# Kernel tuning notes

Measured on AMD Instinct MI355X. Metric: run time of the kernel, lower is better.

## Reference

```python
import jax, jax.numpy as jnp
import numpy as np


def setup_inputs() -> dict:
    key = jax.random.key(0)
    ks = jax.random.split(key, 8)
    B, C, T = 8, 512, 2048
    Cq = C // 8
    s = 0.02
    return {
        "x": jax.random.normal(ks[0], (B, C, T), dtype=jnp.float32),
        "wq": jax.random.normal(ks[1], (Cq, C), dtype=jnp.float32) * s,
        "bq": jax.random.normal(ks[2], (Cq,), dtype=jnp.float32) * s,
        "wk": jax.random.normal(ks[3], (Cq, C), dtype=jnp.float32) * s,
        "bk": jax.random.normal(ks[4], (Cq,), dtype=jnp.float32) * s,
        "wv": jax.random.normal(ks[5], (C, C), dtype=jnp.float32) * s,
        "bv": jax.random.normal(ks[6], (C,), dtype=jnp.float32) * s,
        "gamma": jax.random.normal(ks[7], (1,), dtype=jnp.float32) * s,
    }


def reference(x, wq, bq, wk, bk, wv, bv, gamma):
    # x: [B, C, T]; conv1d with kernel_size=1 == per-timestep linear over channels
    q = jnp.einsum('oc,bct->bto', wq, x) + bq          # [B, T, Cq]
    k = jnp.einsum('oc,bct->bot', wk, x) + bk[None, :, None]  # [B, Cq, T]
    v = jnp.einsum('oc,bct->bto', wv, x) + bv          # [B, T, C]
    attn = jnp.einsum('bto,bos->bts', q, k)            # [B, T, T] (unscaled)
    attn = jax.nn.softmax(attn, axis=-1)
    out = jnp.einsum('bts,bsc->bct', attn, v)          # [B, C, T]
    return gamma[0] * out + x
```

## Files before the change

kernel.cpp:

```cpp
#include <hip/hip_runtime.h>


#define B_ 8
#define C_ 512
#define T_ 2048

typedef __attribute__((ext_vector_type(4))) float f32x4;
typedef __attribute__((ext_vector_type(8))) short bf16x8;
typedef unsigned short u16;
typedef unsigned int u32;

__device__ __forceinline__ u16 f2bf(float f) {
  u32 u = __float_as_uint(f);
  u += 0x7fffu + ((u >> 16) & 1);
  return (u16)(u >> 16);
}
__device__ __forceinline__ float bf2f(u16 h) {
  return __uint_as_float(((u32)h) << 16);
}

extern "C" __global__ __launch_bounds__(256)
void k_wcvt(const float* __restrict__ wq, const float* __restrict__ wk,
            const float* __restrict__ wv, u16* __restrict__ W) {
  int i = blockIdx.x * 256 + threadIdx.x;
  const float* src; u16* dst;
  if (i < 8192)       { src = wq + (size_t)i * 4;            dst = W + (size_t)i * 4; }
  else if (i < 16384) { int j = i - 8192;  src = wk + (size_t)j * 4; dst = W + 32768 + (size_t)j * 4; }
  else                { int j = i - 16384; src = wv + (size_t)j * 4; dst = W + 65536 + (size_t)j * 4; }
  float4 f = *(const float4*)src;
  ushort4 o;
  o.x = f2bf(f.x); o.y = f2bf(f.y); o.z = f2bf(f.z); o.w = f2bf(f.w);
  *(ushort4*)dst = o;
}

extern "C" __global__ __launch_bounds__(256)
void k_xpose(const float* __restrict__ x, u16* __restrict__ xT) {
  __shared__ alignas(16) u16 lds[64 * 72];
  const int tid = threadIdx.x;
  const int t0 = blockIdx.x * 64;
  const int c0 = blockIdx.y * 64;
  const int b  = blockIdx.z;
  const int cr = tid >> 2, tq = tid & 3;
  const float* xp = x + ((size_t)(b * C_ + c0 + cr)) * T_ + t0 + tq * 16;
  u16 vals[16];
#pragma unroll
  for (int q = 0; q < 4; q++) {
    float4 f = *(const float4*)(xp + q * 4);
    vals[q * 4 + 0] = f2bf(f.x);
    vals[q * 4 + 1] = f2bf(f.y);
    vals[q * 4 + 2] = f2bf(f.z);
    vals[q * 4 + 3] = f2bf(f.w);
  }
#pragma unroll
  for (int j = 0; j < 16; j++) lds[(tq * 16 + j) * 72 + cr] = vals[j];
  __syncthreads();
  const int tr = tid >> 2, cq = tid & 3;
  uint4 oa = *(const uint4*)&lds[tr * 72 + cq * 16];
  uint4 ob = *(const uint4*)&lds[tr * 72 + cq * 16 + 8];
  u16* op = xT + ((size_t)(b * T_ + t0 + tr)) * C_ + c0 + cq * 16;
  *(uint4*)op = oa;
  *(uint4*)(op + 8) = ob;
}

extern "C" __global__ __launch_bounds__(256)
void k_qk(const u16* __restrict__ xT, const u16* __restrict__ W,
          const float* __restrict__ bq, const float* __restrict__ bk,
          u16* __restrict__ QK) {
  const int tid = threadIdx.x;
  const int wave = tid >> 6, lane = tid & 63;
  const int quad = lane >> 4, l15 = lane & 15;
  const int id = blockIdx.x;
  const int b  = id & 7;
  const int t0 = (id >> 3) * 32;
  const int n0 = wave * 32;
  f32x4 acc[2][2];
#pragma unroll
  for (int i = 0; i < 2; i++)
#pragma unroll
    for (int j = 0; j < 2; j++) acc[i][j] = (f32x4){0.f, 0.f, 0.f, 0.f};
#pragma unroll
  for (int ks = 0; ks < 16; ks++) {
    bf16x8 af[2], bf[2];
#pragma unroll
    for (int mt = 0; mt < 2; mt++)
      af[mt] = *(const bf16x8*)(xT + ((size_t)(b * T_ + t0 + mt * 16 + l15)) * C_ +
                                ks * 32 + quad * 8);
#pragma unroll
    for (int ntl = 0; ntl < 2; ntl++) {
      const int n = n0 + ntl * 16 + l15;
      const u16* wrow = (n < 64) ? (W + (size_t)n * C_)
                                 : (W + 32768 + (size_t)(n - 64) * C_);
      bf[ntl] = *(const bf16x8*)(wrow + ks * 32 + quad * 8);
    }
#pragma unroll
    for (int mt = 0; mt < 2; mt++)
#pragma unroll
      for (int ntl = 0; ntl < 2; ntl++)
        acc[mt][ntl] = __builtin_amdgcn_mfma_f32_16x16x32_bf16(af[mt], bf[ntl],
                                                               acc[mt][ntl], 0, 0, 0);
  }
#pragma unroll
  for (int ntl = 0; ntl < 2; ntl++) {
    const int n = n0 + ntl * 16 + l15;
    const float bias = (n < 64) ? bq[n] : bk[n - 64];
#pragma unroll
    for (int mt = 0; mt < 2; mt++)
#pragma unroll
      for (int r = 0; r < 4; r++) {
        const int t = t0 + mt * 16 + quad * 4 + r;
        QK[((size_t)(b * T_ + t)) * 128 + n] = f2bf(acc[mt][ntl][r] + bias);
      }
  }
}

extern "C" __global__ __launch_bounds__(256)
void k_vt(const u16* __restrict__ xT, const u16* __restrict__ Wv,
          const float* __restrict__ bv, u16* __restrict__ VT) {
  const int tid = threadIdx.x;
  const int wave = tid >> 6, lane = tid & 63;
  const int quad = lane >> 4, l15 = lane & 15;
  const int id = blockIdx.x;
  const int b   = id & 7;
  const int slot = id >> 3;
  const int tt0 = (slot & 15) * 128;
  const int c00 = (slot >> 4) * 128;
  const int wm = (wave >> 1) * 64, wn = (wave & 1) * 64;
  f32x4 acc[4][4];
#pragma unroll
  for (int i = 0; i < 4; i++)
#pragma unroll
    for (int j = 0; j < 4; j++) acc[i][j] = (f32x4){0.f, 0.f, 0.f, 0.f};

  bf16x8 af[2][4], bfr[2][4];
  auto ldst = [&](int ks, int s) {
#pragma unroll
    for (int mt = 0; mt < 4; mt++)
      af[s][mt] = *(const bf16x8*)(Wv + ((size_t)(c00 + wm + mt * 16 + l15)) * C_ +
                                   ks * 32 + quad * 8);
#pragma unroll
    for (int nt = 0; nt < 4; nt++)
      bfr[s][nt] = *(const bf16x8*)(xT + ((size_t)(b * T_ + tt0 + wn + nt * 16 + l15)) * C_ +
                                    ks * 32 + quad * 8);
  };
  ldst(0, 0);
#pragma unroll
  for (int ks = 0; ks < 16; ks++) {
    const int cur = ks & 1;
    if (ks < 15) ldst(ks + 1, cur ^ 1);
#pragma unroll
    for (int mt = 0; mt < 4; mt++)
#pragma unroll
      for (int nt = 0; nt < 4; nt++)
        acc[mt][nt] = __builtin_amdgcn_mfma_f32_16x16x32_bf16(af[cur][mt], bfr[cur][nt],
                                                              acc[mt][nt], 0, 0, 0);
  }
#pragma unroll
  for (int mt = 0; mt < 4; mt++) {
#pragma unroll
    for (int r = 0; r < 4; r++) {
      const int c = c00 + wm + mt * 16 + quad * 4 + r;
      const float bias = bv[c];
#pragma unroll
      for (int nt = 0; nt < 4; nt++) {
        const int t = tt0 + wn + nt * 16 + l15;
        VT[((size_t)(b * C_ + c)) * T_ + t] = f2bf(acc[mt][nt][r] + bias);
      }
    }
  }
}

extern "C" __global__ __launch_bounds__(256)
void k_attn(const u16* __restrict__ QK, const u16* __restrict__ VT,
            const float* __restrict__ x, const float* __restrict__ gamma,
            float* __restrict__ out) {
  __shared__ alignas(16) u16 Vt[2][128 * 88];
  __shared__ alignas(16) u16 Pscr[4][32 * 64];

  const int tid = threadIdx.x;
  const int wave = tid >> 6, lane = tid & 63;
  const int quad = lane >> 4, l15 = lane & 15;
  const int id = blockIdx.x;
  const int b  = id & 7;
  const int slot = id >> 3;
  const int c0 = (slot >> 4) * 128;
  const int t0 = (slot & 15) * 128;
  const int t0w = t0 + wave * 32;

  bf16x8 qa[2][2];
#pragma unroll
  for (int mt = 0; mt < 2; mt++) {
    const u16* qp = QK + ((size_t)(b * T_ + t0w + mt * 16 + l15)) * 128 + quad * 8;
    qa[mt][0] = *(const bf16x8*)qp;
    qa[mt][1] = *(const bf16x8*)(qp + 32);
  }
  f32x4 acc[2][8];
#pragma unroll
  for (int i = 0; i < 2; i++)
#pragma unroll
    for (int j = 0; j < 8; j++) acc[i][j] = (f32x4){0.f, 0.f, 0.f, 0.f};
  f32x4 acc1[2];
  acc1[0] = (f32x4){0.f, 0.f, 0.f, 0.f};
  acc1[1] = (f32x4){0.f, 0.f, 0.f, 0.f};
  bf16x8 ones;
#pragma unroll
  for (int j = 0; j < 8; j++) ones[j] = (short)0x3F80;

  const u16* vbase = VT + ((size_t)(b * C_ + c0)) * T_;
  const u16* kp = QK + ((size_t)(b * T_ + l15)) * 128 + 64 + quad * 8;

  const int vrow = tid >> 1, vh = tid & 1;
  uint4 vreg[4];
  auto gl_v = [&](int s0) {
    const u16* p = vbase + (size_t)vrow * T_ + s0 + vh * 32;
    vreg[0] = *(const uint4*)p;
    vreg[1] = *(const uint4*)(p + 8);
    vreg[2] = *(const uint4*)(p + 16);
    vreg[3] = *(const uint4*)(p + 24);
  };
  auto st_v = [&](int par) {
    u16* d = &Vt[par][vrow * 88 + vh * 32];
    *(uint4*)(d)      = vreg[0];
    *(uint4*)(d + 8)  = vreg[1];
    *(uint4*)(d + 16) = vreg[2];
    *(uint4*)(d + 24) = vreg[3];
  };

  bf16x8 kbf[4][2];
  auto ld_k = [&](int s0) {
#pragma unroll
    for (int nt = 0; nt < 4; nt++)
#pragma unroll
      for (int ks = 0; ks < 2; ks++)
        kbf[nt][ks] = *(const bf16x8*)(kp + (size_t)((s0 + nt * 16) << 7) + ks * 32);
  };

  ld_k(0);
  gl_v(0);
  st_v(0);
  __syncthreads();

  for (int i = 0; i < 32; i++) {
    const int par = i & 1;
    if (i < 31) gl_v((i + 1) * 64);

    f32x4 sacc[2][4];
#pragma unroll
    for (int mt = 0; mt < 2; mt++)
#pragma unroll
      for (int nt = 0; nt < 4; nt++) sacc[mt][nt] = (f32x4){0.f, 0.f, 0.f, 0.f};
#pragma unroll
    for (int nt = 0; nt < 4; nt++)
#pragma unroll
      for (int ks = 0; ks < 2; ks++)
#pragma unroll
        for (int mt = 0; mt < 2; mt++)
          sacc[mt][nt] = __builtin_amdgcn_mfma_f32_16x16x32_bf16(qa[mt][ks], kbf[nt][ks],
                                                                 sacc[mt][nt], 0, 0, 0);

    if (i < 31) ld_k((i + 1) * 64);

#pragma unroll
    for (int mt = 0; mt < 2; mt++)
#pragma unroll
      for (int nt = 0; nt < 4; nt++) {
        float p0 = __expf(sacc[mt][nt][0]);
        float p1 = __expf(sacc[mt][nt][1]);
        float p2 = __expf(sacc[mt][nt][2]);
        float p3 = __expf(sacc[mt][nt][3]);
        u32 w01, w23;
        asm("v_cvt_pk_bf16_f32 %0, %1, %2" : "=v"(w01) : "v"(p0), "v"(p1));
        asm("v_cvt_pk_bf16_f32 %0, %1, %2" : "=v"(w23) : "v"(p2), "v"(p3));
        const u16 h[4] = {(u16)w01, (u16)(w01 >> 16), (u16)w23, (u16)(w23 >> 16)};
        const int sH = (nt << 1) | (l15 >> 3);
        const int sL = l15 & 7;
#pragma unroll
        for (int r = 0; r < 4; r++) {
          const int tl = mt * 16 + quad * 4 + r;
          Pscr[wave][tl * 64 + ((sH ^ (tl & 7)) << 3) + sL] = h[r];
        }
      }
    bf16x8 pa[2][2];
#pragma unroll
    for (int mt = 0; mt < 2; mt++)
#pragma unroll
      for (int sb = 0; sb < 2; sb++) {
        const int tl = mt * 16 + l15;
        const int sl = ((sb * 4 + quad) ^ (tl & 7)) << 3;
        pa[mt][sb] = *(const bf16x8*)&Pscr[wave][tl * 64 + sl];
      }

#pragma unroll
    for (int mt = 0; mt < 2; mt++)
#pragma unroll
      for (int sb = 0; sb < 2; sb++)
        acc1[mt] = __builtin_amdgcn_mfma_f32_16x16x32_bf16(pa[mt][sb], ones,
                                                           acc1[mt], 0, 0, 0);

#pragma unroll
    for (int nt = 0; nt < 8; nt++)
#pragma unroll
      for (int sb = 0; sb < 2; sb++) {
        bf16x8 vb = *(const bf16x8*)&Vt[par][(nt * 16 + l15) * 88 + sb * 32 + quad * 8];
#pragma unroll
        for (int mt = 0; mt < 2; mt++)
          acc[mt][nt] = __builtin_amdgcn_mfma_f32_16x16x32_bf16(pa[mt][sb], vb,
                                                                acc[mt][nt], 0, 0, 0);
      }

    if (i < 31) st_v(par ^ 1);
    __syncthreads();
  }

  const float g = gamma[0];
#pragma unroll
  for (int mt = 0; mt < 2; mt++) {
#pragma unroll
    for (int r = 0; r < 4; r++) {
      const int t = t0w + mt * 16 + quad * 4 + r;
      const float sc = g / acc1[mt][r];
#pragma unroll
      for (int nt = 0; nt < 8; nt++) {
        const int c = c0 + nt * 16 + l15;
        const size_t idx = ((size_t)(b * C_ + c)) * T_ + t;
        out[idx] = acc[mt][nt][r] * sc + x[idx];
      }
    }
  }
}

extern "C" void kernel_launch(void* const* d_in, const int* in_sizes, int n_in,
                              void* d_out, int out_size, void* d_ws, size_t ws_size,
                              hipStream_t stream) {
  (void)in_sizes; (void)n_in; (void)out_size; (void)ws_size;
  const float* x  = (const float*)d_in[0];
  const float* wq = (const float*)d_in[1];
  const float* bq = (const float*)d_in[2];
  const float* wk = (const float*)d_in[3];
  const float* bk = (const float*)d_in[4];
  const float* wv = (const float*)d_in[5];
  const float* bv = (const float*)d_in[6];
  const float* gm = (const float*)d_in[7];
  float* out = (float*)d_out;

  u16* xT = (u16*)d_out;
  u16* Wb = (u16*)((char*)d_out + (size_t)17 * 1024 * 1024);
  char* ws = (char*)d_ws;
  u16* QK = (u16*)ws;
  u16* VT = (u16*)(ws + (size_t)4 * 1024 * 1024);

  k_wcvt<<<320, 256, 0, stream>>>(wq, wk, wv, Wb);
  k_xpose<<<dim3(32, 8, 8), 256, 0, stream>>>(x, xT);
  k_qk  <<<512, 256, 0, stream>>>(xT, Wb, bq, bk, QK);
  k_vt  <<<512, 256, 0, stream>>>(xT, Wb + 65536, bv, VT);
  k_attn<<<512, 256, 0, stream>>>(QK, VT, x, gm, out);
}
```

Measured before the change: 257.0 us.

## Switch attention to 32x32x16 MFMA with transposed S and register-resident P

Rewrites the attention kernel around 32x32x16 bf16 MFMAs. S is computed transposed (K as the A operand) so that the exp'd probabilities can be repacked into B-operand fragments in registers with v_permlane32_swap, which removes the per-wave LDS scratch round trip for P. The row-sum now accumulates in a scalar plus one cross-half shuffle instead of extra MFMAs against a ones vector. The V tile in LDS drops its padding in favour of an XOR swizzle. Together these cut LDS traffic and instruction count, but the larger accumulators raise register pressure and the output stores change their access pattern.

```diff
diff --git a/kernel.cpp b/kernel.cpp
--- a/kernel.cpp
+++ b/kernel.cpp
@@ -6,6 +6,7 @@
 #define T_ 2048
 
 typedef __attribute__((ext_vector_type(4))) float f32x4;
+typedef __attribute__((ext_vector_type(16))) float f32x16;
 typedef __attribute__((ext_vector_type(8))) short bf16x8;
 typedef unsigned short u16;
 typedef unsigned int u32;
@@ -173,12 +174,11 @@
 void k_attn(const u16* __restrict__ QK, const u16* __restrict__ VT,
             const float* __restrict__ x, const float* __restrict__ gamma,
             float* __restrict__ out) {
-  __shared__ alignas(16) u16 Vt[2][128 * 88];
-  __shared__ alignas(16) u16 Pscr[4][32 * 64];
+  __shared__ alignas(16) u16 Vt[2][128 * 64];
 
   const int tid = threadIdx.x;
   const int wave = tid >> 6, lane = tid & 63;
-  const int quad = lane >> 4, l15 = lane & 15;
+  const int l31 = lane & 31, lh = lane >> 5;
   const int id = blockIdx.x;
   const int b  = id & 7;
   const int slot = id >> 3;
@@ -186,27 +186,21 @@
   const int t0 = (slot & 15) * 128;
   const int t0w = t0 + wave * 32;
 
-  bf16x8 qa[2][2];
-#pragma unroll
-  for (int mt = 0; mt < 2; mt++) {
-    const u16* qp = QK + ((size_t)(b * T_ + t0w + mt * 16 + l15)) * 128 + quad * 8;
-    qa[mt][0] = *(const bf16x8*)qp;
-    qa[mt][1] = *(const bf16x8*)(qp + 32);
-  }
-  f32x4 acc[2][8];
-#pragma unroll
-  for (int i = 0; i < 2; i++)
-#pragma unroll
-    for (int j = 0; j < 8; j++) acc[i][j] = (f32x4){0.f, 0.f, 0.f, 0.f};
-  f32x4 acc1[2];
-  acc1[0] = (f32x4){0.f, 0.f, 0.f, 0.f};
-  acc1[1] = (f32x4){0.f, 0.f, 0.f, 0.f};
-  bf16x8 ones;
-#pragma unroll
-  for (int j = 0; j < 8; j++) ones[j] = (short)0x3F80;
+  bf16x8 qf[4];
+  {
+    const u16* qq = QK + ((size_t)(b * T_ + t0w + l31)) * 128 + lh * 8;
+#pragma unroll
+    for (int kc = 0; kc < 4; kc++)
+      qf[kc] = *(const bf16x8*)(qq + kc * 16);
+  }
+
+  f32x16 acc[4];
+#pragma unroll
+  for (int ct = 0; ct < 4; ct++) acc[ct] = {};
+  float lacc = 0.f;
 
   const u16* vbase = VT + ((size_t)(b * C_ + c0)) * T_;
-  const u16* kp = QK + ((size_t)(b * T_ + l15)) * 128 + 64 + quad * 8;
+  const u16* kq = QK + ((size_t)(b * T_ + l31)) * 128 + 64 + lh * 8;
 
   const int vrow = tid >> 1, vh = tid & 1;
   uint4 vreg[4];
@@ -218,20 +212,19 @@
     vreg[3] = *(const uint4*)(p + 24);
   };
   auto st_v = [&](int par) {
-    u16* d = &Vt[par][vrow * 88 + vh * 32];
-    *(uint4*)(d)      = vreg[0];
-    *(uint4*)(d + 8)  = vreg[1];
-    *(uint4*)(d + 16) = vreg[2];
-    *(uint4*)(d + 24) = vreg[3];
+    u16* row = &Vt[par][vrow * 64];
+#pragma unroll
+    for (int k = 0; k < 4; k++)
+      *(uint4*)(row + (((vh * 4 + k) ^ (vrow & 7)) << 3)) = vreg[k];
   };
 
-  bf16x8 kbf[4][2];
+  bf16x8 kbf[2][4];
   auto ld_k = [&](int s0) {
 #pragma unroll
-    for (int nt = 0; nt < 4; nt++)
-#pragma unroll
-      for (int ks = 0; ks < 2; ks++)
-        kbf[nt][ks] = *(const bf16x8*)(kp + (size_t)((s0 + nt * 16) << 7) + ks * 32);
+    for (int nt = 0; nt < 2; nt++)
+#pragma unroll
+      for (int kc = 0; kc < 4; kc++)
+        kbf[nt][kc] = *(const bf16x8*)(kq + (size_t)((s0 + nt * 32) << 7) + kc * 16);
   };
 
   ld_k(0);
@@ -243,87 +236,65 @@
     const int par = i & 1;
     if (i < 31) gl_v((i + 1) * 64);
 
-    f32x4 sacc[2][4];
-#pragma unroll
-    for (int mt = 0; mt < 2; mt++)
-#pragma unroll
-      for (int nt = 0; nt < 4; nt++) sacc[mt][nt] = (f32x4){0.f, 0.f, 0.f, 0.f};
-#pragma unroll
-    for (int nt = 0; nt < 4; nt++)
-#pragma unroll
-      for (int ks = 0; ks < 2; ks++)
-#pragma unroll
-        for (int mt = 0; mt < 2; mt++)
-          sacc[mt][nt] = __builtin_amdgcn_mfma_f32_16x16x32_bf16(qa[mt][ks], kbf[nt][ks],
-                                                                 sacc[mt][nt], 0, 0, 0);
+    bf16x8 pf[4];
+#pragma unroll
+    for (int nt = 0; nt < 2; nt++) {
+      f32x16 s = {};
+#pragma unroll
+      for (int kc = 0; kc < 4; kc++)
+        s = __builtin_amdgcn_mfma_f32_32x32x16_bf16(kbf[nt][kc], qf[kc], s, 0, 0, 0);
+      float p[16];
+#pragma unroll
+      for (int r = 0; r < 16; r++) {
+        p[r] = __expf(s[r]);
+        lacc += p[r];
+      }
+#pragma unroll
+      for (int g = 0; g < 2; g++) {
+        const float* pp = p + g * 8;
+        u32 A, Bv, Cv, Dv;
+        asm("v_cvt_pk_bf16_f32 %0, %1, %2" : "=v"(A)  : "v"(pp[0]), "v"(pp[1]));
+        asm("v_cvt_pk_bf16_f32 %0, %1, %2" : "=v"(Bv) : "v"(pp[2]), "v"(pp[3]));
+        asm("v_cvt_pk_bf16_f32 %0, %1, %2" : "=v"(Cv) : "v"(pp[4]), "v"(pp[5]));
+        asm("v_cvt_pk_bf16_f32 %0, %1, %2" : "=v"(Dv) : "v"(pp[6]), "v"(pp[7]));
+        asm("v_permlane32_swap_b32 %0, %1" : "+v"(A), "+v"(Cv));
+        asm("v_permlane32_swap_b32 %0, %1" : "+v"(Bv), "+v"(Dv));
+        union { bf16x8 v; u32 w[4]; } u;
+        u.w[0] = A; u.w[1] = Bv; u.w[2] = Cv; u.w[3] = Dv;
+        pf[nt * 2 + g] = u.v;
+      }
+    }
 
     if (i < 31) ld_k((i + 1) * 64);
 
 #pragma unroll
-    for (int mt = 0; mt < 2; mt++)
-#pragma unroll
-      for (int nt = 0; nt < 4; nt++) {
-        float p0 = __expf(sacc[mt][nt][0]);
-        float p1 = __expf(sacc[mt][nt][1]);
-        float p2 = __expf(sacc[mt][nt][2]);
-        float p3 = __expf(sacc[mt][nt][3]);
-        u32 w01, w23;
-        asm("v_cvt_pk_bf16_f32 %0, %1, %2" : "=v"(w01) : "v"(p0), "v"(p1));
-        asm("v_cvt_pk_bf16_f32 %0, %1, %2" : "=v"(w23) : "v"(p2), "v"(p3));
-        const u16 h[4] = {(u16)w01, (u16)(w01 >> 16), (u16)w23, (u16)(w23 >> 16)};
-        const int sH = (nt << 1) | (l15 >> 3);
-        const int sL = l15 & 7;
-#pragma unroll
-        for (int r = 0; r < 4; r++) {
-          const int tl = mt * 16 + quad * 4 + r;
-          Pscr[wave][tl * 64 + ((sH ^ (tl & 7)) << 3) + sL] = h[r];
-        }
-      }
-    bf16x8 pa[2][2];
-#pragma unroll
-    for (int mt = 0; mt < 2; mt++)
-#pragma unroll
-      for (int sb = 0; sb < 2; sb++) {
-        const int tl = mt * 16 + l15;
-        const int sl = ((sb * 4 + quad) ^ (tl & 7)) << 3;
-        pa[mt][sb] = *(const bf16x8*)&Pscr[wave][tl * 64 + sl];
-      }
-
-#pragma unroll
-    for (int mt = 0; mt < 2; mt++)
-#pragma unroll
-      for (int sb = 0; sb < 2; sb++)
-        acc1[mt] = __builtin_amdgcn_mfma_f32_16x16x32_bf16(pa[mt][sb], ones,
-                                                           acc1[mt], 0, 0, 0);
-
-#pragma unroll
-    for (int nt = 0; nt < 8; nt++)
-#pragma unroll
-      for (int sb = 0; sb < 2; sb++) {
-        bf16x8 vb = *(const bf16x8*)&Vt[par][(nt * 16 + l15) * 88 + sb * 32 + quad * 8];
-#pragma unroll
-        for (int mt = 0; mt < 2; mt++)
-          acc[mt][nt] = __builtin_amdgcn_mfma_f32_16x16x32_bf16(pa[mt][sb], vb,
-                                                                acc[mt][nt], 0, 0, 0);
-      }
+    for (int ct = 0; ct < 4; ct++) {
+      const int cl = ct * 32 + l31;
+      const u16* vrowp = &Vt[par][cl * 64];
+      const int swz = cl & 7;
+#pragma unroll
+      for (int kc = 0; kc < 4; kc++) {
+        bf16x8 vb = *(const bf16x8*)(vrowp + ((((kc << 1) | lh) ^ swz) << 3));
+        acc[ct] = __builtin_amdgcn_mfma_f32_32x32x16_bf16(vb, pf[kc], acc[ct], 0, 0, 0);
+      }
+    }
 
     if (i < 31) st_v(par ^ 1);
     __syncthreads();
   }
 
+  const float den = lacc + __shfl_xor(lacc, 32);
   const float g = gamma[0];
-#pragma unroll
-  for (int mt = 0; mt < 2; mt++) {
-#pragma unroll
-    for (int r = 0; r < 4; r++) {
-      const int t = t0w + mt * 16 + quad * 4 + r;
-      const float sc = g / acc1[mt][r];
-#pragma unroll
-      for (int nt = 0; nt < 8; nt++) {
-        const int c = c0 + nt * 16 + l15;
-        const size_t idx = ((size_t)(b * C_ + c)) * T_ + t;
-        out[idx] = acc[mt][nt][r] * sc + x[idx];
-      }
+  const float sc = g / den;
+
+  const int t = t0w + l31;
+#pragma unroll
+  for (int ct = 0; ct < 4; ct++) {
+#pragma unroll
+    for (int r = 0; r < 16; r++) {
+      const int c = c0 + ct * 32 + (r & 3) + 8 * (r >> 2) + 4 * lh;
+      const size_t idx = ((size_t)(b * C_ + c)) * T_ + t;
+      out[idx] = acc[ct][r] * sc + x[idx];
     }
   }
 }
```

Measured after the change: 286.6 us. +11.5%, slower.

## Software-pipeline QK^T of next tile with softmax/PV of current tile

Applied to the files above, without the earlier changes.

Restructures the attention loop so the QK^T MFMAs for tile i+1 are issued before the exp/P-scratch/PV work for tile i, using two ping-ponged score register sets. The loop is unrolled by two to alternate the buffers, with a prologue and epilogue. This is meant to hide MFMA and LDS latency across stages, at the cost of more live registers, which may lower occupancy.

```diff
diff --git a/kernel.cpp b/kernel.cpp
--- a/kernel.cpp
+++ b/kernel.cpp
@@ -234,39 +234,30 @@
         kbf[nt][ks] = *(const bf16x8*)(kp + (size_t)((s0 + nt * 16) << 7) + ks * 32);
   };
 
-  ld_k(0);
-  gl_v(0);
-  st_v(0);
-  __syncthreads();
-
-  for (int i = 0; i < 32; i++) {
-    const int par = i & 1;
-    if (i < 31) gl_v((i + 1) * 64);
-
-    f32x4 sacc[2][4];
-#pragma unroll
-    for (int mt = 0; mt < 2; mt++)
-#pragma unroll
-      for (int nt = 0; nt < 4; nt++) sacc[mt][nt] = (f32x4){0.f, 0.f, 0.f, 0.f};
+  auto qkt = [&](f32x4 (&S)[2][4]) {
+#pragma unroll
+    for (int mt = 0; mt < 2; mt++)
+#pragma unroll
+      for (int nt = 0; nt < 4; nt++) S[mt][nt] = (f32x4){0.f, 0.f, 0.f, 0.f};
 #pragma unroll
     for (int nt = 0; nt < 4; nt++)
 #pragma unroll
       for (int ks = 0; ks < 2; ks++)
 #pragma unroll
         for (int mt = 0; mt < 2; mt++)
-          sacc[mt][nt] = __builtin_amdgcn_mfma_f32_16x16x32_bf16(qa[mt][ks], kbf[nt][ks],
-                                                                 sacc[mt][nt], 0, 0, 0);
-
-    if (i < 31) ld_k((i + 1) * 64);
-
+          S[mt][nt] = __builtin_amdgcn_mfma_f32_16x16x32_bf16(qa[mt][ks], kbf[nt][ks],
+                                                              S[mt][nt], 0, 0, 0);
+  };
+
+  auto smpv = [&](f32x4 (&S)[2][4], int rbuf) {
 #pragma unroll
     for (int mt = 0; mt < 2; mt++)
 #pragma unroll
       for (int nt = 0; nt < 4; nt++) {
-        float p0 = __expf(sacc[mt][nt][0]);
-        float p1 = __expf(sacc[mt][nt][1]);
-        float p2 = __expf(sacc[mt][nt][2]);
-        float p3 = __expf(sacc[mt][nt][3]);
+        float p0 = __expf(S[mt][nt][0]);
+        float p1 = __expf(S[mt][nt][1]);
+        float p2 = __expf(S[mt][nt][2]);
+        float p3 = __expf(S[mt][nt][3]);
         u32 w01, w23;
         asm("v_cvt_pk_bf16_f32 %0, %1, %2" : "=v"(w01) : "v"(p0), "v"(p1));
         asm("v_cvt_pk_bf16_f32 %0, %1, %2" : "=v"(w23) : "v"(p2), "v"(p3));
@@ -288,28 +279,50 @@
         const int sl = ((sb * 4 + quad) ^ (tl & 7)) << 3;
         pa[mt][sb] = *(const bf16x8*)&Pscr[wave][tl * 64 + sl];
       }
-
 #pragma unroll
     for (int mt = 0; mt < 2; mt++)
 #pragma unroll
       for (int sb = 0; sb < 2; sb++)
         acc1[mt] = __builtin_amdgcn_mfma_f32_16x16x32_bf16(pa[mt][sb], ones,
                                                            acc1[mt], 0, 0, 0);
-
 #pragma unroll
     for (int nt = 0; nt < 8; nt++)
 #pragma unroll
       for (int sb = 0; sb < 2; sb++) {
-        bf16x8 vb = *(const bf16x8*)&Vt[par][(nt * 16 + l15) * 88 + sb * 32 + quad * 8];
+        bf16x8 vb = *(const bf16x8*)&Vt[rbuf][(nt * 16 + l15) * 88 + sb * 32 + quad * 8];
 #pragma unroll
         for (int mt = 0; mt < 2; mt++)
           acc[mt][nt] = __builtin_amdgcn_mfma_f32_16x16x32_bf16(pa[mt][sb], vb,
                                                                 acc[mt][nt], 0, 0, 0);
       }
-
-    if (i < 31) st_v(par ^ 1);
+  };
+
+  f32x4 sA[2][4], sB[2][4];
+
+  auto body = [&](int i, f32x4 (&SW)[2][4], f32x4 (&SR)[2][4], bool ldk_next) {
+    const int wbuf = i & 1;
+    gl_v(i * 64);
+    qkt(SW);
+    if (ldk_next) ld_k((i + 1) * 64);
+    smpv(SR, wbuf ^ 1);
+    st_v(wbuf);
     __syncthreads();
-  }
+  };
+
+  ld_k(0);
+  gl_v(0);
+  st_v(0);
+  __syncthreads();
+  qkt(sA);
+  ld_k(64);
+
+  for (int ii = 1; ii <= 29; ii += 2) {
+    body(ii,     sB, sA, true);
+    body(ii + 1, sA, sB, true);
+  }
+  body(31, sB, sA, false);
+
+  smpv(sB, 1);
 
   const float g = gamma[0];
 #pragma unroll
```

New measurement: 302.1 us. 17.5% more time.

## Merge prep/projection launches and stage V tiles via direct global-to-LDS loads

Applied to the files above, without the earlier changes.

The weight conversion and x transpose are merged into one launch, and the Q/K and V projections into another, cutting five kernel launches to three and letting independent blocks run side by side. In the attention kernel, V tiles are now copied with global_load_lds straight into an XOR-swizzled, unpadded LDS buffer instead of passing through registers. The aim is to remove launch gaps and register pressure from the V staging, and to overlap that copy with compute. The cost is a dependency on the swizzle indexing being correct and on how the async LDS writes are ordered against the existing barrier.

```diff
diff --git a/kernel.cpp b/kernel.cpp
--- a/kernel.cpp
+++ b/kernel.cpp
@@ -20,151 +20,149 @@
 }
 
 extern "C" __global__ __launch_bounds__(256)
-void k_wcvt(const float* __restrict__ wq, const float* __restrict__ wk,
+void k_prep(const float* __restrict__ x, u16* __restrict__ xT,
+            const float* __restrict__ wq, const float* __restrict__ wk,
             const float* __restrict__ wv, u16* __restrict__ W) {
-  int i = blockIdx.x * 256 + threadIdx.x;
-  const float* src; u16* dst;
-  if (i < 8192)       { src = wq + (size_t)i * 4;            dst = W + (size_t)i * 4; }
-  else if (i < 16384) { int j = i - 8192;  src = wk + (size_t)j * 4; dst = W + 32768 + (size_t)j * 4; }
-  else                { int j = i - 16384; src = wv + (size_t)j * 4; dst = W + 65536 + (size_t)j * 4; }
-  float4 f = *(const float4*)src;
-  ushort4 o;
-  o.x = f2bf(f.x); o.y = f2bf(f.y); o.z = f2bf(f.z); o.w = f2bf(f.w);
-  *(ushort4*)dst = o;
+  __shared__ alignas(16) u16 lds[64 * 72];
+  const int bid = blockIdx.x;
+  const int tid = threadIdx.x;
+  if (bid < 2048) {
+    const int t0 = (bid & 31) * 64;
+    const int c0 = ((bid >> 5) & 7) * 64;
+    const int b  = (bid >> 8) & 7;
+    const int cr = tid >> 2, tq = tid & 3;
+    const float* xp = x + ((size_t)(b * C_ + c0 + cr)) * T_ + t0 + tq * 16;
+    u16 vals[16];
+#pragma unroll
+    for (int q = 0; q < 4; q++) {
+      float4 f = *(const float4*)(xp + q * 4);
+      vals[q * 4 + 0] = f2bf(f.x);
+      vals[q * 4 + 1] = f2bf(f.y);
+      vals[q * 4 + 2] = f2bf(f.z);
+      vals[q * 4 + 3] = f2bf(f.w);
+    }
+#pragma unroll
+    for (int j = 0; j < 16; j++) lds[(tq * 16 + j) * 72 + cr] = vals[j];
+    __syncthreads();
+    const int tr = tid >> 2, cq = tid & 3;
+    uint4 oa = *(const uint4*)&lds[tr * 72 + cq * 16];
+    uint4 ob = *(const uint4*)&lds[tr * 72 + cq * 16 + 8];
+    u16* op = xT + ((size_t)(b * T_ + t0 + tr)) * C_ + c0 + cq * 16;
+    *(uint4*)op = oa;
+    *(uint4*)(op + 8) = ob;
+  } else {
+    int i = (bid - 2048) * 256 + tid;
+    const float* src; u16* dst;
+    if (i < 8192)       { src = wq + (size_t)i * 4;            dst = W + (size_t)i * 4; }
+    else if (i < 16384) { int j = i - 8192;  src = wk + (size_t)j * 4; dst = W + 32768 + (size_t)j * 4; }
+    else                { int j = i - 16384; src = wv + (size_t)j * 4; dst = W + 65536 + (size_t)j * 4; }
+    float4 f = *(const float4*)src;
+    ushort4 o;
+    o.x = f2bf(f.x); o.y = f2bf(f.y); o.z = f2bf(f.z); o.w = f2bf(f.w);
+    *(ushort4*)dst = o;
+  }
 }
 
 extern "C" __global__ __launch_bounds__(256)
-void k_xpose(const float* __restrict__ x, u16* __restrict__ xT) {
-  __shared__ alignas(16) u16 lds[64 * 72];
-  const int tid = threadIdx.x;
-  const int t0 = blockIdx.x * 64;
-  const int c0 = blockIdx.y * 64;
-  const int b  = blockIdx.z;
-  const int cr = tid >> 2, tq = tid & 3;
-  const float* xp = x + ((size_t)(b * C_ + c0 + cr)) * T_ + t0 + tq * 16;
-  u16 vals[16];
-#pragma unroll
-  for (int q = 0; q < 4; q++) {
-    float4 f = *(const float4*)(xp + q * 4);
-    vals[q * 4 + 0] = f2bf(f.x);
-    vals[q * 4 + 1] = f2bf(f.y);
-    vals[q * 4 + 2] = f2bf(f.z);
-    vals[q * 4 + 3] = f2bf(f.w);
-  }
-#pragma unroll
-  for (int j = 0; j < 16; j++) lds[(tq * 16 + j) * 72 + cr] = vals[j];
-  __syncthreads();
-  const int tr = tid >> 2, cq = tid & 3;
-  uint4 oa = *(const uint4*)&lds[tr * 72 + cq * 16];
-  uint4 ob = *(const uint4*)&lds[tr * 72 + cq * 16 + 8];
-  u16* op = xT + ((size_t)(b * T_ + t0 + tr)) * C_ + c0 + cq * 16;
-  *(uint4*)op = oa;
-  *(uint4*)(op + 8) = ob;
-}
-
-extern "C" __global__ __launch_bounds__(256)
-void k_qk(const u16* __restrict__ xT, const u16* __restrict__ W,
-          const float* __restrict__ bq, const float* __restrict__ bk,
-          u16* __restrict__ QK) {
+void k_proj(const u16* __restrict__ xT, const u16* __restrict__ W,
+            const float* __restrict__ bq, const float* __restrict__ bk,
+            const float* __restrict__ bv, u16* __restrict__ QK,
+            u16* __restrict__ VT) {
   const int tid = threadIdx.x;
   const int wave = tid >> 6, lane = tid & 63;
   const int quad = lane >> 4, l15 = lane & 15;
-  const int id = blockIdx.x;
-  const int b  = id & 7;
-  const int t0 = (id >> 3) * 32;
-  const int n0 = wave * 32;
-  f32x4 acc[2][2];
-#pragma unroll
-  for (int i = 0; i < 2; i++)
-#pragma unroll
-    for (int j = 0; j < 2; j++) acc[i][j] = (f32x4){0.f, 0.f, 0.f, 0.f};
-#pragma unroll
-  for (int ks = 0; ks < 16; ks++) {
-    bf16x8 af[2], bf[2];
-#pragma unroll
-    for (int mt = 0; mt < 2; mt++)
-      af[mt] = *(const bf16x8*)(xT + ((size_t)(b * T_ + t0 + mt * 16 + l15)) * C_ +
-                                ks * 32 + quad * 8);
+  if (blockIdx.x < 512) {
+    const u16* Wv = W + 65536;
+    const int id = blockIdx.x;
+    const int b   = id & 7;
+    const int slot = id >> 3;
+    const int tt0 = (slot & 15) * 128;
+    const int c00 = (slot >> 4) * 128;
+    const int wm = (wave >> 1) * 64, wn = (wave & 1) * 64;
+    f32x4 acc[4][4];
+#pragma unroll
+    for (int i = 0; i < 4; i++)
+#pragma unroll
+      for (int j = 0; j < 4; j++) acc[i][j] = (f32x4){0.f, 0.f, 0.f, 0.f};
+
+    bf16x8 af[2][4], bfr[2][4];
+    auto ldst = [&](int ks, int s) {
+#pragma unroll
+      for (int mt = 0; mt < 4; mt++)
+        af[s][mt] = *(const bf16x8*)(Wv + ((size_t)(c00 + wm + mt * 16 + l15)) * C_ +
+                                     ks * 32 + quad * 8);
+#pragma unroll
+      for (int nt = 0; nt < 4; nt++)
+        bfr[s][nt] = *(const bf16x8*)(xT + ((size_t)(b * T_ + tt0 + wn + nt * 16 + l15)) * C_ +
+                                      ks * 32 + quad * 8);
+    };
+    ldst(0, 0);
+#pragma unroll
+    for (int ks = 0; ks < 16; ks++) {
+      const int cur = ks & 1;
+      if (ks < 15) ldst(ks + 1, cur ^ 1);
+#pragma unroll
+      for (int mt = 0; mt < 4; mt++)
+#pragma unroll
+        for (int nt = 0; nt < 4; nt++)
+          acc[mt][nt] = __builtin_amdgcn_mfma_f32_16x16x32_bf16(af[cur][mt], bfr[cur][nt],
+                                                                acc[mt][nt], 0, 0, 0);
+    }
+#pragma unroll
+    for (int mt = 0; mt < 4; mt++) {
+#pragma unroll
+      for (int r = 0; r < 4; r++) {
+        const int c = c00 + wm + mt * 16 + quad * 4 + r;
+        const float bias = bv[c];
+#pragma unroll
+        for (int nt = 0; nt < 4; nt++) {
+          const int t = tt0 + wn + nt * 16 + l15;
+          VT[((size_t)(b * C_ + c)) * T_ + t] = f2bf(acc[mt][nt][r] + bias);
+        }
+      }
+    }
+  } else {
+    const int id = blockIdx.x - 512;
+    const int b  = id & 7;
+    const int t0 = (id >> 3) * 32;
+    const int n0 = wave * 32;
+    f32x4 acc[2][2];
+#pragma unroll
+    for (int i = 0; i < 2; i++)
+#pragma unroll
+      for (int j = 0; j < 2; j++) acc[i][j] = (f32x4){0.f, 0.f, 0.f, 0.f};
+#pragma unroll
+    for (int ks = 0; ks < 16; ks++) {
+      bf16x8 af[2], bf[2];
+#pragma unroll
+      for (int mt = 0; mt < 2; mt++)
+        af[mt] = *(const bf16x8*)(xT + ((size_t)(b * T_ + t0 + mt * 16 + l15)) * C_ +
+                                  ks * 32 + quad * 8);
+#pragma unroll
+      for (int ntl = 0; ntl < 2; ntl++) {
+        const int n = n0 + ntl * 16 + l15;
+        const u16* wrow = (n < 64) ? (W + (size_t)n * C_)
+                                   : (W + 32768 + (size_t)(n - 64) * C_);
+        bf[ntl] = *(const bf16x8*)(wrow + ks * 32 + quad * 8);
+      }
+#pragma unroll
+      for (int mt = 0; mt < 2; mt++)
+#pragma unroll
+        for (int ntl = 0; ntl < 2; ntl++)
+          acc[mt][ntl] = __builtin_amdgcn_mfma_f32_16x16x32_bf16(af[mt], bf[ntl],
+                                                                 acc[mt][ntl], 0, 0, 0);
+    }
 #pragma unroll
     for (int ntl = 0; ntl < 2; ntl++) {
       const int n = n0 + ntl * 16 + l15;
-      const u16* wrow = (n < 64) ? (W + (size_t)n * C_)
-                                 : (W + 32768 + (size_t)(n - 64) * C_);
-      bf[ntl] = *(const bf16x8*)(wrow + ks * 32 + quad * 8);
-    }
-#pragma unroll
-    for (int mt = 0; mt < 2; mt++)
-#pragma unroll
-      for (int ntl = 0; ntl < 2; ntl++)
-        acc[mt][ntl] = __builtin_amdgcn_mfma_f32_16x16x32_bf16(af[mt], bf[ntl],
-                                                               acc[mt][ntl], 0, 0, 0);
-  }
-#pragma unroll
-  for (int ntl = 0; ntl < 2; ntl++) {
-    const int n = n0 + ntl * 16 + l15;
-    const float bias = (n < 64) ? bq[n] : bk[n - 64];
-#pragma unroll
-    for (int mt = 0; mt < 2; mt++)
-#pragma unroll
-      for (int r = 0; r < 4; r++) {
-        const int t = t0 + mt * 16 + quad * 4 + r;
-        QK[((size_t)(b * T_ + t)) * 128 + n] = f2bf(acc[mt][ntl][r] + bias);
-      }
-  }
-}
-
-extern "C" __global__ __launch_bounds__(256)
-void k_vt(const u16* __restrict__ xT, const u16* __restrict__ Wv,
-          const float* __restrict__ bv, u16* __restrict__ VT) {
-  const int tid = threadIdx.x;
-  const int wave = tid >> 6, lane = tid & 63;
-  const int quad = lane >> 4, l15 = lane & 15;
-  const int id = blockIdx.x;
-  const int b   = id & 7;
-  const int slot = id >> 3;
-  const int tt0 = (slot & 15) * 128;
-  const int c00 = (slot >> 4) * 128;
-  const int wm = (wave >> 1) * 64, wn = (wave & 1) * 64;
-  f32x4 acc[4][4];
-#pragma unroll
-  for (int i = 0; i < 4; i++)
-#pragma unroll
-    for (int j = 0; j < 4; j++) acc[i][j] = (f32x4){0.f, 0.f, 0.f, 0.f};
-
-  bf16x8 af[2][4], bfr[2][4];
-  auto ldst = [&](int ks, int s) {
-#pragma unroll
-    for (int mt = 0; mt < 4; mt++)
-      af[s][mt] = *(const bf16x8*)(Wv + ((size_t)(c00 + wm + mt * 16 + l15)) * C_ +
-                                   ks * 32 + quad * 8);
-#pragma unroll
-    for (int nt = 0; nt < 4; nt++)
-      bfr[s][nt] = *(const bf16x8*)(xT + ((size_t)(b * T_ + tt0 + wn + nt * 16 + l15)) * C_ +
-                                    ks * 32 + quad * 8);
-  };
-  ldst(0, 0);
-#pragma unroll
-  for (int ks = 0; ks < 16; ks++) {
-    const int cur = ks & 1;
-    if (ks < 15) ldst(ks + 1, cur ^ 1);
-#pragma unroll
-    for (int mt = 0; mt < 4; mt++)
-#pragma unroll
-      for (int nt = 0; nt < 4; nt++)
-        acc[mt][nt] = __builtin_amdgcn_mfma_f32_16x16x32_bf16(af[cur][mt], bfr[cur][nt],
-                                                              acc[mt][nt], 0, 0, 0);
-  }
-#pragma unroll
-  for (int mt = 0; mt < 4; mt++) {
-#pragma unroll
-    for (int r = 0; r < 4; r++) {
-      const int c = c00 + wm + mt * 16 + quad * 4 + r;
-      const float bias = bv[c];
-#pragma unroll
-      for (int nt = 0; nt < 4; nt++) {
-        const int t = tt0 + wn + nt * 16 + l15;
-        VT[((size_t)(b * C_ + c)) * T_ + t] = f2bf(acc[mt][nt][r] + bias);
-      }
+      const float bias = (n < 64) ? bq[n] : bk[n - 64];
+#pragma unroll
+      for (int mt = 0; mt < 2; mt++)
+#pragma unroll
+        for (int r = 0; r < 4; r++) {
+          const int t = t0 + mt * 16 + quad * 4 + r;
+          QK[((size_t)(b * T_ + t)) * 128 + n] = f2bf(acc[mt][ntl][r] + bias);
+        }
     }
   }
 }
@@ -173,7 +171,7 @@
 void k_attn(const u16* __restrict__ QK, const u16* __restrict__ VT,
             const float* __restrict__ x, const float* __restrict__ gamma,
             float* __restrict__ out) {
-  __shared__ alignas(16) u16 Vt[2][128 * 88];
+  __shared__ alignas(16) u16 Vt[2][128 * 64];
   __shared__ alignas(16) u16 Pscr[4][32 * 64];
 
   const int tid = threadIdx.x;
@@ -208,21 +206,17 @@
   const u16* vbase = VT + ((size_t)(b * C_ + c0)) * T_;
   const u16* kp = QK + ((size_t)(b * T_ + l15)) * 128 + 64 + quad * 8;
 
-  const int vrow = tid >> 1, vh = tid & 1;
-  uint4 vreg[4];
-  auto gl_v = [&](int s0) {
-    const u16* p = vbase + (size_t)vrow * T_ + s0 + vh * 32;
-    vreg[0] = *(const uint4*)p;
-    vreg[1] = *(const uint4*)(p + 8);
-    vreg[2] = *(const uint4*)(p + 16);
-    vreg[3] = *(const uint4*)(p + 24);
-  };
-  auto st_v = [&](int par) {
-    u16* d = &Vt[par][vrow * 88 + vh * 32];
-    *(uint4*)(d)      = vreg[0];
-    *(uint4*)(d + 8)  = vreg[1];
-    *(uint4*)(d + 16) = vreg[2];
-    *(uint4*)(d + 24) = vreg[3];
+  const int vlr = lane >> 3, vlc = lane & 7;
+  auto stage_v = [&](int s0, int par) {
+#pragma unroll
+    for (int j = 0; j < 4; j++) {
+      const int row = wave * 32 + j * 8 + vlr;
+      const u16* src = vbase + (size_t)row * T_ + s0 + ((vlc ^ vlr) << 3);
+      u16* dst = &Vt[par][(wave * 32 + j * 8) * 64];
+      __builtin_amdgcn_global_load_lds(
+          (const __attribute__((address_space(1))) void*)src,
+          (__attribute__((address_space(3))) void*)dst, 16, 0, 0);
+    }
   };
 
   bf16x8 kbf[4][2];
@@ -235,13 +229,12 @@
   };
 
   ld_k(0);
-  gl_v(0);
-  st_v(0);
+  stage_v(0, 0);
   __syncthreads();
 
   for (int i = 0; i < 32; i++) {
     const int par = i & 1;
-    if (i < 31) gl_v((i + 1) * 64);
+    if (i < 31) stage_v((i + 1) * 64, par ^ 1);
 
     f32x4 sacc[2][4];
 #pragma unroll
@@ -300,14 +293,15 @@
     for (int nt = 0; nt < 8; nt++)
 #pragma unroll
       for (int sb = 0; sb < 2; sb++) {
-        bf16x8 vb = *(const bf16x8*)&Vt[par][(nt * 16 + l15) * 88 + sb * 32 + quad * 8];
+        const int row = nt * 16 + l15;
+        bf16x8 vb = *(const bf16x8*)&Vt[par][row * 64 +
+                                             (((sb * 4 + quad) ^ (l15 & 7)) << 3)];
 #pragma unroll
         for (int mt = 0; mt < 2; mt++)
           acc[mt][nt] = __builtin_amdgcn_mfma_f32_16x16x32_bf16(pa[mt][sb], vb,
                                                                 acc[mt][nt], 0, 0, 0);
       }
 
-    if (i < 31) st_v(par ^ 1);
     __syncthreads();
   }
 
@@ -348,9 +342,7 @@
   u16* QK = (u16*)ws;
   u16* VT = (u16*)(ws + (size_t)4 * 1024 * 1024);
 
-  k_wcvt<<<320, 256, 0, stream>>>(wq, wk, wv, Wb);
-  k_xpose<<<dim3(32, 8, 8), 256, 0, stream>>>(x, xT);
-  k_qk  <<<512, 256, 0, stream>>>(xT, Wb, bq, bk, QK);
-  k_vt  <<<512, 256, 0, stream>>>(xT, Wb + 65536, bv, VT);
+  k_prep<<<2368, 256, 0, stream>>>(x, xT, wq, wk, wv, Wb);
+  k_proj<<<1024, 256, 0, stream>>>(xT, Wb, bq, bk, bv, QK, VT);
   k_attn<<<512, 256, 0, stream>>>(QK, VT, x, gm, out);
 }
```

Result: faster. 240.2 us (-6.5%).
